# Performance work log

Hardware: AMD Instinct MI355X
Metric: run time of the kernel (lower is better)

The kernel has to match this reference:

```python
import jax, jax.numpy as jnp
import numpy as np

D_MODEL = 1024
N_HEADS = 16
D_K = D_MODEL // N_HEADS
THETA = 10000.0
BATCH, SEQ = 2, 2048


def setup_inputs() -> dict:
    key = jax.random.key(0)
    k1, k2, k3 = jax.random.split(key, 3)
    std_qkv = float(np.sqrt(2.0 / (3 * D_MODEL + D_MODEL)))
    std_o = float(np.sqrt(2.0 / (D_MODEL + D_MODEL)))
    return {
        "x": jax.random.normal(k1, (BATCH, SEQ, D_MODEL), dtype=jnp.float32),
        "w_qkv": jax.random.normal(k2, (3 * D_MODEL, D_MODEL), dtype=jnp.float32) * std_qkv,
        "w_o": jax.random.normal(k3, (D_MODEL, D_MODEL), dtype=jnp.float32) * std_o,
        "token_positions": jnp.arange(SEQ, dtype=jnp.int32),
    }


def _rope(x, token_positions):
    # x: [..., s, d_k]; interleaved rotary embedding
    d_k = x.shape[-1]
    freqs = jnp.arange(0, d_k, 2, dtype=jnp.float32) / d_k          # [d_k/2]
    inv_freqs = 1.0 / (THETA ** freqs)
    angles = token_positions.astype(jnp.float32)[:, None] * inv_freqs  # [s, d_k/2]
    cos, sin = jnp.cos(angles), jnp.sin(angles)
    x_even, x_odd = x[..., 0::2], x[..., 1::2]
    rot_even = x_even * cos - x_odd * sin
    rot_odd = x_even * sin + x_odd * cos
    # interleave back: out[..., 2i] = rot_even[i], out[..., 2i+1] = rot_odd[i]
    return jnp.stack([rot_even, rot_odd], axis=-1).reshape(x.shape)


def reference(x, w_qkv, w_o, token_positions):
    b, s, _ = x.shape
    qkv = jnp.einsum('oi,bsi->bso', w_qkv, x)                        # [b, s, 3*d_model]
    q, k, v = jnp.split(qkv, 3, axis=-1)
    def to_heads(t):
        return t.reshape(b, s, N_HEADS, D_K).transpose(0, 2, 1, 3)  # [b, h, s, d]
    q, k, v = to_heads(q), to_heads(k), to_heads(v)
    q = _rope(q, token_positions)
    k = _rope(k, token_positions)
    scores = jnp.einsum('bhqd,bhkd->bhqk', q, k) / jnp.sqrt(jnp.float32(D_K))
    causal = jnp.tril(jnp.ones((s, s), dtype=bool))
    scores = jnp.where(causal, scores, -jnp.inf)
    attn = jax.nn.softmax(scores, axis=-1)
    y = jnp.einsum('bhqk,bhkd->bhqd', attn, v)
    y = y.transpose(0, 2, 1, 3).reshape(b, s, D_MODEL)
    return jnp.einsum('oi,bsi->bso', w_o, y)
```

## Files before the change

kernel.cpp:

```cpp
#include <hip/hip_runtime.h>
#include <math.h>

#define DEV __device__ __forceinline__

typedef __attribute__((ext_vector_type(8))) short bf16x8;
typedef __attribute__((ext_vector_type(4))) float f32x4;
typedef __attribute__((ext_vector_type(4))) unsigned int u32x4;

typedef __attribute__((address_space(3))) unsigned int lds_u32;
typedef const __attribute__((address_space(1))) unsigned int glb_u32;

DEV void gload16(const unsigned short* g, unsigned short* l) {
  __builtin_amdgcn_global_load_lds((glb_u32*)g, (lds_u32*)l, 16, 0, 0);
}

DEV bf16x8 lds_read8(const unsigned short* base, unsigned int byteoff) {
  return *reinterpret_cast<const bf16x8*>(
      reinterpret_cast<const char*>(base) + byteoff);
}

DEV float fexp2(float x) { return __builtin_amdgcn_exp2f(x); }

DEV unsigned short f2bf(float f) {
  union { float f; unsigned int u; } v; v.f = f;
  unsigned int u = v.u;
  unsigned int r = (u + 0x7fffu + ((u >> 16) & 1u)) >> 16;
  return (unsigned short)r;
}
DEV float bf2f(unsigned short h) {
  union { unsigned int u; float f; } v; v.u = ((unsigned int)h) << 16;
  return v.f;
}
DEV unsigned int cvtpk_bf16(float lo, float hi) {
  unsigned int r;
  asm("v_cvt_pk_bf16_f32 %0, %1, %2" : "=v"(r) : "v"(lo), "v"(hi));
  return r;
}

__global__ void cvt_f32_bf16(const float* __restrict__ in,
                             unsigned short* __restrict__ out, int n4) {
  int stride = gridDim.x * blockDim.x;
  for (int i = blockIdx.x * blockDim.x + threadIdx.x; i < n4; i += stride) {
    float4 f = reinterpret_cast<const float4*>(in)[i];
    ushort4 o;
    o.x = f2bf(f.x); o.y = f2bf(f.y); o.z = f2bf(f.z); o.w = f2bf(f.w);
    reinterpret_cast<ushort4*>(out)[i] = o;
  }
}

__global__ void cvt2_f32_bf16(const float* __restrict__ ina,
                              unsigned short* __restrict__ outa, int n4a,
                              const float* __restrict__ inb,
                              unsigned short* __restrict__ outb, int n4b) {
  int stride = gridDim.x * blockDim.x;
  int total = n4a + n4b;
  for (int i = blockIdx.x * blockDim.x + threadIdx.x; i < total; i += stride) {
    if (i < n4a) {
      float4 f = reinterpret_cast<const float4*>(ina)[i];
      ushort4 o;
      o.x = f2bf(f.x); o.y = f2bf(f.y); o.z = f2bf(f.z); o.w = f2bf(f.w);
      reinterpret_cast<ushort4*>(outa)[i] = o;
    } else {
      int j = i - n4a;
      float4 f = reinterpret_cast<const float4*>(inb)[j];
      ushort4 o;
      o.x = f2bf(f.x); o.y = f2bf(f.y); o.z = f2bf(f.z); o.w = f2bf(f.w);
      reinterpret_cast<ushort4*>(outb)[j] = o;
    }
  }
}


#define GEMM_PROLOGUE(A_, B_, K_)                                              \
  __shared__ unsigned short Ab[2][4096];                                       \
  __shared__ unsigned short Bb[2][4096];                                       \
  const int tid = threadIdx.x;                                                 \
  const int lane = tid & 63, wid = tid >> 6;                                   \
  const int wm = (wid >> 1) * 64, wn = (wid & 1) * 64;                         \
  const int fr = lane & 15, kq = lane >> 4;                                    \
  const int arow0 = blockIdx.x * 128;                                          \
  const int brow0 = blockIdx.y * 128;                                          \
  const int srow = wid * 16 + (lane >> 2);                                     \
  const int sslot = (((lane & 3) ^ ((lane >> 2) & 3))) * 8;                    \
  const unsigned short* aptr = (A_) + (size_t)(arow0 + srow) * (K_) + sslot;   \
  const unsigned short* bptr = (B_) + (size_t)(brow0 + srow) * (K_) + sslot;   \
  unsigned int offa[4], offb[4];                                               \
  _Pragma("unroll") for (int i = 0; i < 4; i++) {                              \
    offa[i] = (unsigned)((wm + i * 16 + fr) * 64 + ((kq ^ (fr & 3)) * 16));    \
    offb[i] = (unsigned)((wn + i * 16 + fr) * 64 + ((kq ^ (fr & 3)) * 16));    \
  }                                                                            \
  f32x4 acc[4][4] = {};

#define GSTAGE(BI, K_)                                             \
  {                                                                \
    gload16(aptr, &Ab[BI][wid * 512]);                             \
    gload16(aptr + (size_t)64 * (K_), &Ab[BI][2048 + wid * 512]);  \
    gload16(bptr, &Bb[BI][wid * 512]);                             \
    gload16(bptr + (size_t)64 * (K_), &Bb[BI][2048 + wid * 512]);  \
    aptr += 32;                                                    \
    bptr += 32;                                                    \
  }

#define GCOMP(BI)                                                                      \
  {                                                                                    \
    bf16x8 af[4], bfr[4];                                                              \
    _Pragma("unroll") for (int i = 0; i < 4; i++) af[i] = lds_read8(Ab[BI], offa[i]);  \
    _Pragma("unroll") for (int j = 0; j < 4; j++) bfr[j] = lds_read8(Bb[BI], offb[j]); \
    _Pragma("unroll") for (int i = 0; i < 4; i++)                                      \
      _Pragma("unroll") for (int j = 0; j < 4; j++)                                    \
        acc[i][j] = __builtin_amdgcn_mfma_f32_16x16x32_bf16(af[i], bfr[j], acc[i][j], 0, 0, 0); \
  }

#define GEMM_MAIN(K_)                       \
  {                                         \
    const int nk = (K_) >> 5;     \
    GSTAGE(0, K_);                          \
    for (int ks = 0; ks < nk; ks += 2) {    \
      __syncthreads();                      \
      GSTAGE(1, K_);                        \
      GCOMP(0);                             \
      __syncthreads();                      \
      if (ks + 2 < nk) GSTAGE(0, K_);       \
      GCOMP(1);                             \
    }                                       \
  }

template <bool BF16_OUT>
__global__ __launch_bounds__(256) void gemm_bt(const unsigned short* __restrict__ A,
                                               const unsigned short* __restrict__ B,
                                               void* __restrict__ Cv,
                                               int M, int N, int K) {
  GEMM_PROLOGUE(A, B, K)
  GEMM_MAIN(K)
#pragma unroll
  for (int i = 0; i < 4; i++) {
#pragma unroll
    for (int j = 0; j < 4; j++) {
#pragma unroll
      for (int r = 0; r < 4; r++) {
        size_t row = (size_t)(arow0 + wm + i * 16 + kq * 4 + r);
        size_t col = (size_t)(brow0 + wn + j * 16 + fr);
        if (BF16_OUT)
          ((unsigned short*)Cv)[row * N + col] = f2bf(acc[i][j][r]);
        else
          ((float*)Cv)[row * N + col] = acc[i][j][r];
      }
    }
  }
}

__global__ __launch_bounds__(256) void gemm_qkv(const unsigned short* __restrict__ A,
                                                const unsigned short* __restrict__ B,
                                                unsigned short* __restrict__ qkv,
                                                unsigned short* __restrict__ vt,
                                                int K) {
  const int N = 3072;
  GEMM_PROLOGUE(A, B, K)
  GEMM_MAIN(K)
  if (brow0 < 2048) {
#pragma unroll
    for (int i = 0; i < 4; i++) {
#pragma unroll
      for (int j = 0; j < 4; j++) {
#pragma unroll
        for (int r = 0; r < 4; r++) {
          size_t row = (size_t)(arow0 + wm + i * 16 + kq * 4 + r);
          size_t col = (size_t)(brow0 + wn + j * 16 + fr);
          qkv[row * N + col] = f2bf(acc[i][j][r]);
        }
      }
    }
  } else {
#pragma unroll
    for (int i = 0; i < 4; i++) {
      int row_base = arow0 + wm + i * 16 + kq * 4;
      int b = row_base >> 11;
      int s = row_base & 2047;
      int p_base = (s & ~31) + 8 * ((s >> 2) & 3) + 4 * ((s >> 4) & 1);
#pragma unroll
      for (int j = 0; j < 4; j++) {
        int col = (brow0 - 2048) + wn + j * 16 + fr;
        int bh = b * 16 + (col >> 6);
        int d = col & 63;
        ushort4 o;
        o.x = f2bf(acc[i][j][0]);
        o.y = f2bf(acc[i][j][1]);
        o.z = f2bf(acc[i][j][2]);
        o.w = f2bf(acc[i][j][3]);
        *reinterpret_cast<ushort4*>(&vt[((size_t)bh * 64 + d) * 2048 + p_base]) = o;
      }
    }
  }
}

__global__ __launch_bounds__(256) void rope_kernel(unsigned short* __restrict__ qkv,
                                                   const int* __restrict__ pos) {
  int m = blockIdx.x;
  int s = m & 2047;
  int t = threadIdx.x;
  __shared__ float Cl[32], Sl[32];
  if (t < 32) {
    float position = (float)pos[s];
    float inv = __expf(-(float)t * (9.210340371976184f / 32.0f));
    float ang = position * inv;
    Cl[t] = cosf(ang);
    Sl[t] = sinf(ang);
  }
  __syncthreads();
  const float QS = 0.18033688011112042f;
  int h = t >> 4, g = t & 15;
  float c0 = Cl[2 * g], s0 = Sl[2 * g], c1 = Cl[2 * g + 1], s1 = Sl[2 * g + 1];
  size_t base = (size_t)m * 3072 + h * 64 + 4 * g;
  ushort4 qv = *reinterpret_cast<ushort4*>(&qkv[base]);
  float qe0 = bf2f(qv.x), qo0 = bf2f(qv.y), qe1 = bf2f(qv.z), qo1 = bf2f(qv.w);
  qv.x = f2bf((qe0 * c0 - qo0 * s0) * QS);
  qv.y = f2bf((qe0 * s0 + qo0 * c0) * QS);
  qv.z = f2bf((qe1 * c1 - qo1 * s1) * QS);
  qv.w = f2bf((qe1 * s1 + qo1 * c1) * QS);
  *reinterpret_cast<ushort4*>(&qkv[base]) = qv;
  size_t kb = base + 1024;
  ushort4 kv = *reinterpret_cast<ushort4*>(&qkv[kb]);
  float ke0 = bf2f(kv.x), ko0 = bf2f(kv.y), ke1 = bf2f(kv.z), ko1 = bf2f(kv.w);
  kv.x = f2bf(ke0 * c0 - ko0 * s0);
  kv.y = f2bf(ke0 * s0 + ko0 * c0);
  kv.z = f2bf(ke1 * c1 - ko1 * s1);
  kv.w = f2bf(ke1 * s1 + ko1 * c1);
  *reinterpret_cast<ushort4*>(&qkv[kb]) = kv;
}

__global__ __launch_bounds__(256, 4) void attn_kernel(const unsigned short* __restrict__ qkv,
                                                      const unsigned short* __restrict__ vt,
                                                      unsigned short* __restrict__ Y) {
  int bid = blockIdx.x;
  int bh = bid & 31;
  int qt = 31 - (bid >> 5);
  int h = bh & 15, b = bh >> 4;
  int tid = threadIdx.x, lane = tid & 63, wid = tid >> 6;
  int fr = lane & 15, kq = lane >> 4;
  int qbase = qt * 64 + wid * 16;

  const size_t mrow0 = (size_t)b * 2048;
  const unsigned short* Qp = qkv + (mrow0 + qbase) * 3072 + h * 64;
  const unsigned short* Kp = qkv + mrow0 * 3072 + 1024 + h * 64;
  const unsigned short* Vp = vt + ((size_t)bh * 64) * 2048;

  __shared__ unsigned short Klds[2][4096];
  __shared__ unsigned short Vlds[2][4096];

  bf16x8 qf[2];
#pragma unroll
  for (int ks = 0; ks < 2; ks++)
    qf[ks] = *reinterpret_cast<const bf16x8*>(&Qp[(size_t)fr * 3072 + ks * 32 + kq * 8]);

  const int srow = tid >> 3;
  const int schunk = (tid & 7) ^ (srow & 7);
  const unsigned short* kstage = Kp + (size_t)srow * 3072 + schunk * 8;
  const unsigned short* vstage = Vp + (size_t)srow * 2048 + schunk * 8;

  unsigned int offk[8], offv[8];
#pragma unroll
  for (int g = 0; g < 4; g++)
#pragma unroll
    for (int ks = 0; ks < 2; ks++) {
      int R = g * 16 + fr;
      offk[g * 2 + ks] = (unsigned)(R * 128 + (((4 * ks + kq) ^ (R & 7)) * 16));
    }
#pragma unroll
  for (int db = 0; db < 4; db++)
#pragma unroll
    for (int hf = 0; hf < 2; hf++) {
      int d = db * 16 + fr;
      offv[db * 2 + hf] = (unsigned)(d * 128 + (((4 * hf + kq) ^ (d & 7)) * 16));
    }

  f32x4 acc[4] = {};
  float mr = -1e30f, lr = 0.0f;
  const int q_lane = qbase + fr;
  const int ntiles = qt + 1;

#define STAGE(BI)                                                     \
  {                                                                   \
    gload16(kstage, &Klds[BI][wid * 512]);                            \
    gload16(kstage + (size_t)32 * 3072, &Klds[BI][2048 + wid * 512]); \
    gload16(vstage, &Vlds[BI][wid * 512]);                            \
    gload16(vstage + 32 * 2048, &Vlds[BI][2048 + wid * 512]);         \
    kstage += (size_t)64 * 3072;                                      \
    vstage += 64;                                                     \
  }

#define TILE_COMPUTE(T, BI)                                                           \
  {                                                                                   \
    const int t_ = (T);                                                               \
    const bool masked_ = (t_ == qt);                                                  \
    f32x4 sc[4] = {};                                                                 \
    __builtin_amdgcn_s_setprio(1);                                                    \
    _Pragma("unroll") for (int g = 0; g < 4; g++) {                                   \
      _Pragma("unroll") for (int ks = 0; ks < 2; ks++) {                              \
        bf16x8 kf = lds_read8(Klds[BI], offk[g * 2 + ks]);                            \
        sc[g] = __builtin_amdgcn_mfma_f32_16x16x32_bf16(kf, qf[ks], sc[g], 0, 0, 0);  \
      }                                                                               \
    }                                                                                 \
    __builtin_amdgcn_s_setprio(0);                                                    \
    float s[16];                                                                      \
    _Pragma("unroll") for (int g = 0; g < 4; g++)                                     \
      _Pragma("unroll") for (int r = 0; r < 4; r++) {                                 \
        float v = sc[g][r];                                                           \
        if (masked_) {                                                                \
          int k = t_ * 64 + g * 16 + kq * 4 + r;                                      \
          if (k > q_lane) v = -1e30f;                                                 \
        }                                                                             \
        s[g * 4 + r] = v;                                                             \
      }                                                                               \
    float t0 = fmaxf(fmaxf(s[0], s[1]), s[2]);                                        \
    float t1 = fmaxf(fmaxf(s[3], s[4]), s[5]);                                        \
    float t2 = fmaxf(fmaxf(s[6], s[7]), s[8]);                                        \
    float t3 = fmaxf(fmaxf(s[9], s[10]), s[11]);                                      \
    float t4 = fmaxf(fmaxf(s[12], s[13]), s[14]);                                     \
    float u0 = fmaxf(fmaxf(t0, t1), t2);                                              \
    float u1 = fmaxf(fmaxf(t3, t4), s[15]);                                           \
    float rm = fmaxf(u0, u1);                                                         \
    if (!__all(rm <= mr + 8.0f)) {                                                    \
      float rmf = fmaxf(rm, __shfl_xor(rm, 16));                                      \
      rmf = fmaxf(rmf, __shfl_xor(rmf, 32));                                          \
      float mn = fmaxf(mr, rmf);                                                      \
      float scl = fexp2(mr - mn);                                                     \
      mr = mn;                                                                        \
      lr *= scl;                                                                      \
      _Pragma("unroll") for (int db = 0; db < 4; db++)                                \
        _Pragma("unroll") for (int r = 0; r < 4; r++) acc[db][r] *= scl;              \
    }                                                                                 \
    _Pragma("unroll") for (int i = 0; i < 16; i++) s[i] = fexp2(s[i] - mr);           \
    float a8[8];                                                                      \
    _Pragma("unroll") for (int i = 0; i < 8; i++) a8[i] = s[2 * i] + s[2 * i + 1];    \
    lr += ((a8[0] + a8[1]) + (a8[2] + a8[3])) + ((a8[4] + a8[5]) + (a8[6] + a8[7]));  \
    u32x4 W0 = {cvtpk_bf16(s[0], s[1]), cvtpk_bf16(s[2], s[3]),                       \
                cvtpk_bf16(s[4], s[5]), cvtpk_bf16(s[6], s[7])};                      \
    u32x4 W1 = {cvtpk_bf16(s[8], s[9]), cvtpk_bf16(s[10], s[11]),                     \
                cvtpk_bf16(s[12], s[13]), cvtpk_bf16(s[14], s[15])};                  \
    bf16x8 pa0 = *reinterpret_cast<bf16x8*>(&W0);                                     \
    bf16x8 pa1 = *reinterpret_cast<bf16x8*>(&W1);                                     \
    __builtin_amdgcn_s_setprio(1);                                                    \
    _Pragma("unroll") for (int db = 0; db < 4; db++) {                                \
      bf16x8 vf0 = lds_read8(Vlds[BI], offv[db * 2]);                                 \
      acc[db] = __builtin_amdgcn_mfma_f32_16x16x32_bf16(vf0, pa0, acc[db], 0, 0, 0);  \
      bf16x8 vf1 = lds_read8(Vlds[BI], offv[db * 2 + 1]);                             \
      acc[db] = __builtin_amdgcn_mfma_f32_16x16x32_bf16(vf1, pa1, acc[db], 0, 0, 0);  \
    }                                                                                 \
    __builtin_amdgcn_s_setprio(0);                                                    \
  }

  STAGE(0);
  for (int t = 0; t < ntiles; t += 2) {
    __syncthreads();
    if (t + 1 < ntiles) STAGE(1);
    TILE_COMPUTE(t, 0);
    if (t + 1 >= ntiles) break;
    __syncthreads();
    if (t + 2 < ntiles) STAGE(0);
    TILE_COMPUTE(t + 1, 1);
  }
#undef TILE_COMPUTE
#undef STAGE

  lr += __shfl_xor(lr, 16);
  lr += __shfl_xor(lr, 32);
  float inv = 1.0f / lr;
  unsigned short* yp = Y + (mrow0 + qbase + fr) * 1024 + h * 64 + kq * 4;
#pragma unroll
  for (int db = 0; db < 4; db++) {
    ushort4 o;
    o.x = f2bf(acc[db][0] * inv);
    o.y = f2bf(acc[db][1] * inv);
    o.z = f2bf(acc[db][2] * inv);
    o.w = f2bf(acc[db][3] * inv);
    *reinterpret_cast<ushort4*>(yp + db * 16) = o;
  }
}

extern "C" void kernel_launch(void* const* d_in, const int* in_sizes, int n_in,
                              void* d_out, int out_size, void* d_ws, size_t ws_size,
                              hipStream_t stream) {
  const float* x     = (const float*)d_in[0];
  const float* w_qkv = (const float*)d_in[1];
  const float* w_o   = (const float*)d_in[2];
  const int*   pos   = (const int*)d_in[3];
  float* out = (float*)d_out;

  unsigned char* ws = (unsigned char*)d_ws;
  unsigned short* x_bf    = (unsigned short*)(ws);
  unsigned short* wqkv_bf = (unsigned short*)(ws + 8388608);
  unsigned short* wo_bf   = (unsigned short*)(ws + 14680064);
  unsigned short* qkv     = (unsigned short*)(ws + 16777216);
  unsigned short* vt      = (unsigned short*)(ws + 41943040);
  unsigned short* y       = (unsigned short*)(ws + 50331648);

  cvt_f32_bf16<<<1024, 256, 0, stream>>>(x, x_bf, 4096 * 1024 / 4);
  cvt2_f32_bf16<<<1024, 256, 0, stream>>>(w_qkv, wqkv_bf, 3072 * 1024 / 4,
                                          w_o, wo_bf, 1024 * 1024 / 4);

  gemm_qkv<<<dim3(32, 24), 256, 0, stream>>>(x_bf, wqkv_bf, qkv, vt, 1024);

  rope_kernel<<<4096, 256, 0, stream>>>(qkv, pos);

  attn_kernel<<<1024, 256, 0, stream>>>(qkv, vt, y);

  gemm_bt<false><<<dim3(32, 8), 256, 0, stream>>>(y, wo_bf, (void*)out, 4096, 1024, 1024);
}
```

Before: 126.5 us.

## Replace QKV GEMM with 256x256 8-wave pipelined kernel and separate V transpose

Replaces the 128x128 QKV projection GEMM with a 256x256-tile, 512-thread kernel. It uses a larger shared-memory double buffer, staged async global-to-LDS loads interleaved with MFMA phases, setprio hints and a block-swizzled tile order. The permuted V-transpose write moves out of the GEMM epilogue into a new vtrans_kernel that reads V back from qkv. The aim is more data reuse per tile and better load/compute overlap. The cost is one extra kernel launch plus an extra read and write of V, and only 192 blocks, which may underfill the GPU.

Result: faster. 116.0 us (-8.3%).

```diff
diff --git a/kernel.cpp b/kernel.cpp
--- a/kernel.cpp
+++ b/kernel.cpp
@@ -70,6 +70,122 @@
   }
 }
 
+__global__ __launch_bounds__(512, 2) void gemm8_qkv(const unsigned short* __restrict__ A,
+                                                    const unsigned short* __restrict__ B,
+                                                    unsigned short* __restrict__ C) {
+  constexpr int K = 1024;
+  constexpr int NK = 16;
+  __shared__ unsigned short Ls[2][32768];
+
+  const int tid = threadIdx.x;
+  const int lane = tid & 63, wid = tid >> 6;
+  const int wm = (wid >> 2) * 128;
+  const int wn = (wid & 3) * 64;
+  const int fr = lane & 15, kq = lane >> 4;
+
+  int bid = blockIdx.x;
+  int swz = (bid & 7) * 24 + (bid >> 3);
+  int tm = swz & 15, tn = swz >> 4;
+  const int arow0 = tm * 256, brow0 = tn * 256;
+
+  const int subrow = lane >> 3;
+  const int scol = ((lane & 7) ^ subrow) * 8;
+  const unsigned short* aSrc = A + (size_t)(arow0 + wid * 8 + subrow) * K + scol;
+  const unsigned short* bSrc = B + (size_t)(brow0 + wid * 8 + subrow) * K + scol;
+
+  unsigned aoff[2], boff[2];
+#pragma unroll
+  for (int ks = 0; ks < 2; ks++) {
+    unsigned x = ((unsigned)((ks * 4 + kq) ^ (fr & 7))) * 16;
+    aoff[ks] = (unsigned)((wm + fr) * 128) + x;
+    boff[ks] = 32768u + (unsigned)((wn + fr) * 128) + x;
+  }
+
+  f32x4 acc[8][4] = {};
+
+#define STAGE_A8(BUF, H, T)                                                  \
+  {                                                                          \
+    gload16(aSrc + (size_t)((H) * 128) * K + (T) * 64,                       \
+            &Ls[BUF][((H) * 128 + wid * 8) * 64]);                           \
+    gload16(aSrc + (size_t)((H) * 128 + 64) * K + (T) * 64,                  \
+            &Ls[BUF][((H) * 128 + 64 + wid * 8) * 64]);                      \
+  }
+#define STAGE_B8(BUF, H, T)                                                  \
+  {                                                                          \
+    gload16(bSrc + (size_t)((H) * 128) * K + (T) * 64,                       \
+            &Ls[BUF][16384 + ((H) * 128 + wid * 8) * 64]);                   \
+    gload16(bSrc + (size_t)((H) * 128 + 64) * K + (T) * 64,                  \
+            &Ls[BUF][16384 + ((H) * 128 + 64 + wid * 8) * 64]);              \
+  }
+
+  STAGE_A8(0, 0, 0) STAGE_A8(0, 1, 0)
+  STAGE_B8(0, 0, 0) STAGE_B8(0, 1, 0)
+  STAGE_B8(1, 0, 1) STAGE_B8(1, 1, 1)
+  asm volatile("s_waitcnt vmcnt(4)" ::: "memory");
+  __builtin_amdgcn_s_barrier();
+
+#define PHASE8(BUF, P, DO_STAGE)                                              \
+  {                                                                           \
+    bf16x8 af[2][2];                                                          \
+    _Pragma("unroll") for (int mm = 0; mm < 2; mm++)                          \
+      _Pragma("unroll") for (int ks = 0; ks < 2; ks++)                        \
+        af[mm][ks] = lds_read8(Ls[BUF], aoff[ks] + ((P) * 2 + mm) * 2048);    \
+    DO_STAGE                                                                  \
+    __builtin_amdgcn_s_setprio(1);                                            \
+    _Pragma("unroll") for (int mm = 0; mm < 2; mm++)                          \
+      _Pragma("unroll") for (int j = 0; j < 4; j++)                           \
+        _Pragma("unroll") for (int ks = 0; ks < 2; ks++)                      \
+          acc[(P) * 2 + mm][j] = __builtin_amdgcn_mfma_f32_16x16x32_bf16(     \
+              af[mm][ks], bq[j][ks], acc[(P) * 2 + mm][j], 0, 0, 0);          \
+    __builtin_amdgcn_s_setprio(0);                                            \
+  }
+
+#define TILE8(T, BUF)                                                          \
+  {                                                                            \
+    bf16x8 bq[4][2];                                                           \
+    _Pragma("unroll") for (int j = 0; j < 4; j++)                              \
+      _Pragma("unroll") for (int ks = 0; ks < 2; ks++)                         \
+        bq[j][ks] = lds_read8(Ls[BUF], boff[ks] + j * 2048);                   \
+    PHASE8(BUF, 0, {                                                           \
+      if ((T) + 1 < NK) { STAGE_A8(BUF ^ 1, 0, (T) + 1) STAGE_A8(BUF ^ 1, 1, (T) + 1) } \
+    })                                                                         \
+    __builtin_amdgcn_s_barrier();                                              \
+    PHASE8(BUF, 1, { if ((T) + 2 < NK) STAGE_B8(BUF, 0, (T) + 2) })            \
+    __builtin_amdgcn_s_barrier();                                              \
+    PHASE8(BUF, 2, { if ((T) + 2 < NK) STAGE_B8(BUF, 1, (T) + 2) })            \
+    __builtin_amdgcn_s_barrier();                                              \
+    PHASE8(BUF, 3, {})                                                         \
+    if ((T) + 2 < NK) {                                                        \
+      asm volatile("s_waitcnt vmcnt(4)" ::: "memory");                         \
+    } else {                                                                   \
+      asm volatile("s_waitcnt vmcnt(0)" ::: "memory");                         \
+    }                                                                          \
+    __builtin_amdgcn_s_barrier();                                              \
+    __builtin_amdgcn_sched_barrier(0);                                         \
+  }
+
+#pragma unroll 1
+  for (int t = 0; t < NK; t += 2) {
+    TILE8(t, 0)
+    TILE8(t + 1, 1)
+  }
+#undef TILE8
+#undef PHASE8
+#undef STAGE_A8
+#undef STAGE_B8
+
+#pragma unroll
+  for (int m = 0; m < 8; m++) {
+#pragma unroll
+    for (int j = 0; j < 4; j++) {
+      size_t row = (size_t)(arow0 + wm + m * 16 + kq * 4);
+      size_t col = (size_t)(brow0 + wn + j * 16 + fr);
+#pragma unroll
+      for (int r = 0; r < 4; r++)
+        C[(row + r) * 3072 + col] = f2bf(acc[m][j][r]);
+    }
+  }
+}
 
 #define GEMM_PROLOGUE(A_, B_, K_)                                              \
   __shared__ unsigned short Ab[2][4096];                                       \
@@ -144,50 +260,6 @@
           ((unsigned short*)Cv)[row * N + col] = f2bf(acc[i][j][r]);
         else
           ((float*)Cv)[row * N + col] = acc[i][j][r];
-      }
-    }
-  }
-}
-
-__global__ __launch_bounds__(256) void gemm_qkv(const unsigned short* __restrict__ A,
-                                                const unsigned short* __restrict__ B,
-                                                unsigned short* __restrict__ qkv,
-                                                unsigned short* __restrict__ vt,
-                                                int K) {
-  const int N = 3072;
-  GEMM_PROLOGUE(A, B, K)
-  GEMM_MAIN(K)
-  if (brow0 < 2048) {
-#pragma unroll
-    for (int i = 0; i < 4; i++) {
-#pragma unroll
-      for (int j = 0; j < 4; j++) {
-#pragma unroll
-        for (int r = 0; r < 4; r++) {
-          size_t row = (size_t)(arow0 + wm + i * 16 + kq * 4 + r);
-          size_t col = (size_t)(brow0 + wn + j * 16 + fr);
-          qkv[row * N + col] = f2bf(acc[i][j][r]);
-        }
-      }
-    }
-  } else {
-#pragma unroll
-    for (int i = 0; i < 4; i++) {
-      int row_base = arow0 + wm + i * 16 + kq * 4;
-      int b = row_base >> 11;
-      int s = row_base & 2047;
-      int p_base = (s & ~31) + 8 * ((s >> 2) & 3) + 4 * ((s >> 4) & 1);
-#pragma unroll
-      for (int j = 0; j < 4; j++) {
-        int col = (brow0 - 2048) + wn + j * 16 + fr;
-        int bh = b * 16 + (col >> 6);
-        int d = col & 63;
-        ushort4 o;
-        o.x = f2bf(acc[i][j][0]);
-        o.y = f2bf(acc[i][j][1]);
-        o.z = f2bf(acc[i][j][2]);
-        o.w = f2bf(acc[i][j][3]);
-        *reinterpret_cast<ushort4*>(&vt[((size_t)bh * 64 + d) * 2048 + p_base]) = o;
       }
     }
   }
@@ -226,6 +298,40 @@
   kv.z = f2bf(ke1 * c1 - ko1 * s1);
   kv.w = f2bf(ke1 * s1 + ko1 * c1);
   *reinterpret_cast<ushort4*>(&qkv[kb]) = kv;
+}
+
+__global__ __launch_bounds__(256) void vtrans_kernel(const unsigned short* __restrict__ qkv,
+                                                     unsigned short* __restrict__ vt) {
+  int bid = blockIdx.x;
+  int sb = bid & 31;
+  int bh = bid >> 5;
+  int h = bh & 15, b = bh >> 4;
+  __shared__ unsigned short tile[64][72];
+  int t = threadIdx.x;
+  int sl = t >> 2, c0 = (t & 3) * 16;
+  const unsigned short* src = qkv + (size_t)(b * 2048 + sb * 64) * 3072 + 2048 + h * 64;
+  *reinterpret_cast<bf16x8*>(&tile[sl][c0]) =
+      *reinterpret_cast<const bf16x8*>(&src[(size_t)sl * 3072 + c0]);
+  *reinterpret_cast<bf16x8*>(&tile[sl][c0 + 8]) =
+      *reinterpret_cast<const bf16x8*>(&src[(size_t)sl * 3072 + c0 + 8]);
+  __syncthreads();
+  int d = t >> 2, p0 = (t & 3) * 16;
+  unsigned short* dst = vt + ((size_t)bh * 64 + d) * 2048 + sb * 64 + p0;
+  bf16x8 o0, o1;
+#pragma unroll
+  for (int i = 0; i < 8; i++) {
+    int p = p0 + i;
+    int s_in = (p & 32) + ((p >> 2) & 1) * 16 + ((p >> 3) & 3) * 4 + (p & 3);
+    o0[i] = (short)tile[s_in][d];
+  }
+#pragma unroll
+  for (int i = 0; i < 8; i++) {
+    int p = p0 + 8 + i;
+    int s_in = (p & 32) + ((p >> 2) & 1) * 16 + ((p >> 3) & 3) * 4 + (p & 3);
+    o1[i] = (short)tile[s_in][d];
+  }
+  *reinterpret_cast<bf16x8*>(dst) = o0;
+  *reinterpret_cast<bf16x8*>(dst + 8) = o1;
 }
 
 __global__ __launch_bounds__(256, 4) void attn_kernel(const unsigned short* __restrict__ qkv,
@@ -398,9 +504,10 @@
   cvt2_f32_bf16<<<1024, 256, 0, stream>>>(w_qkv, wqkv_bf, 3072 * 1024 / 4,
                                           w_o, wo_bf, 1024 * 1024 / 4);
 
-  gemm_qkv<<<dim3(32, 24), 256, 0, stream>>>(x_bf, wqkv_bf, qkv, vt, 1024);
+  gemm8_qkv<<<192, 512, 0, stream>>>(x_bf, wqkv_bf, qkv);
 
   rope_kernel<<<4096, 256, 0, stream>>>(qkv, pos);
+  vtrans_kernel<<<1024, 256, 0, stream>>>(qkv, vt);
 
   attn_kernel<<<1024, 256, 0, stream>>>(qkv, vt, y);
 
```
